# Optimization experiments

Hardware: AMD Instinct MI355X
Metric: run time of the kernel (lower is better)

## Reference

```python
import jax, jax.numpy as jnp
import numpy as np
from jax import lax

ALPHA = 1.5
DIM = -1
N_ITER = 50


def entmax_bisect(x, alpha=ALPHA, dim=DIM, n_iter=N_ITER):
    # alpha == 1.0 would reduce to softmax; alpha is a static Python float here.
    if alpha == 1.0:
        return jax.nn.softmax(x, axis=dim)
    am1 = alpha - 1.0
    z = x - jnp.max(x, axis=dim, keepdims=True)          # max(z) == 0 along dim
    am1_z = am1 * z
    # torch code sorts z and takes the top element; that equals max(z) == 0, so
    # hi = 0 and lo = hi - 1. We compute the max directly (same math, no sort).
    hi = jnp.max(am1_z, axis=dim, keepdims=True)          # == 0
    lo = hi - 1.0

    inv_am1 = 1.0 / am1

    def sum_probs(tau):
        # sum_i max(0, am1*z_i - tau)^{1/am1}, keepdims
        diff = jnp.maximum(am1_z - tau, 0.0)
        return jnp.sum(jnp.power(diff, inv_am1), axis=dim, keepdims=True)

    # The torch version expands lo downward (up to 64 times) until
    # sum_probs(lo) >= 1 everywhere. Since max(am1_z) == hi, at lo = hi - 1 the
    # argmax element alone contributes (hi - lo)^{1/am1} = 1^{1/am1} = 1, so
    # sum_probs(lo) >= 1 always holds and the torch loop breaks on the first
    # iteration without ever modifying lo. We therefore skip it (identical math).

    def bisect_step(carry, _):
        lo, hi = carry
        mid = (lo + hi) * 0.5
        s = sum_probs(mid)
        lo = jnp.where(s > 1.0, mid, lo)
        hi = jnp.where(s <= 1.0, mid, hi)
        return (lo, hi), None

    (lo, hi), _ = lax.scan(bisect_step, (lo, hi), None, length=n_iter)
    tau_star = (lo + hi) * 0.5
    p = jnp.power(jnp.maximum(am1_z - tau_star, 0.0), inv_am1)
    return p / jnp.maximum(jnp.sum(p, axis=dim, keepdims=True), 1e-12)


def setup_inputs() -> dict:
    key = jax.random.key(0)
    x = jax.random.normal(key, (8, 2048, 2048), dtype=jnp.float32)
    return {"x": x}


def reference(x):
    return entmax_bisect(x, alpha=ALPHA, dim=DIM, n_iter=N_ITER)
```

## Files before the change

### kernel.cpp

```cpp
#include <hip/hip_runtime.h>


constexpr int N = 2048;
constexpr int PER_LANE = N / 64;
constexpr int WAVES_PER_BLOCK = 4;
constexpr int K1 = 6;
constexpr int TOTAL_ITER = 50;
constexpr int BMAX = 8;

__global__ __launch_bounds__(256, 4)
void entmax15_kernel(const float* __restrict__ x,
                     float* __restrict__ out, int rows) {
    __shared__ float s_buf[WAVES_PER_BLOCK][BMAX];
    __shared__ int   s_cnt[WAVES_PER_BLOCK];

    const int wave = threadIdx.x >> 6;
    const int lane = threadIdx.x & 63;
    const int row  = blockIdx.x * WAVES_PER_BLOCK + wave;
    if (row >= rows) return;

    const float4* xr   = reinterpret_cast<const float4*>(x   + (size_t)row * N);
    float4*       outr = reinterpret_cast<float4*>(out + (size_t)row * N);

    float v[PER_LANE];
    #pragma unroll
    for (int c = 0; c < PER_LANE / 4; ++c) {
        float4 t = xr[lane + 64 * c];
        v[4*c+0] = t.x; v[4*c+1] = t.y; v[4*c+2] = t.z; v[4*c+3] = t.w;
    }

    float m = v[0];
    #pragma unroll
    for (int i = 1; i < PER_LANE; ++i) m = fmaxf(m, v[i]);
    #pragma unroll
    for (int off = 32; off >= 1; off >>= 1)
        m = fmaxf(m, __shfl_xor(m, off, 64));

    const float nhm = -0.5f * m;
    #pragma unroll
    for (int i = 0; i < PER_LANE; ++i) v[i] = fmaf(0.5f, v[i], nhm);

    float lo = -1.0f, hi = 0.0f;

    for (int it = 0; it < K1; ++it) {
        const float mid = 0.5f * (lo + hi);
        float s0 = 0.f, s1_ = 0.f, s2_ = 0.f, s3_ = 0.f;
        #pragma unroll
        for (int i = 0; i < PER_LANE; i += 4) {
            float d0 = fmaxf(v[i+0] - mid, 0.f);
            float d1 = fmaxf(v[i+1] - mid, 0.f);
            float d2 = fmaxf(v[i+2] - mid, 0.f);
            float d3 = fmaxf(v[i+3] - mid, 0.f);
            s0 = fmaf(d0, d0, s0); s1_ = fmaf(d1, d1, s1_);
            s2_ = fmaf(d2, d2, s2_); s3_ = fmaf(d3, d3, s3_);
        }
        float s = (s0 + s1_) + (s2_ + s3_);
        #pragma unroll
        for (int off = 32; off >= 1; off >>= 1)
            s += __shfl_xor(s, off, 64);
        if (s > 1.0f) lo = mid; else hi = mid;
    }

    if (lane < BMAX) s_buf[wave][lane] = -1e30f;
    if (lane == 0)   s_cnt[wave] = 0;

    const float cth = hi, lof = lo;
    float nA = 0.f, S1 = 0.f, S2 = 0.f;
    #pragma unroll
    for (int i = 0; i < PER_LANE; ++i) {
        float u  = v[i] - cth;
        float um = fmaxf(u, 0.f);
        nA += (u > 0.f) ? 1.0f : 0.0f;
        S1 += um;
        S2 = fmaf(um, um, S2);
        if (u <= 0.f && v[i] > lof) {
            int k = atomicAdd(&s_cnt[wave], 1);
            if (k < BMAX) s_buf[wave][k] = v[i];
        }
    }
    #pragma unroll
    for (int off = 32; off >= 1; off >>= 1) {
        nA += __shfl_xor(nA, off, 64);
        S1 += __shfl_xor(S1, off, 64);
        S2 += __shfl_xor(S2, off, 64);
    }

    const int cnt = s_cnt[wave];
    float b0 = s_buf[wave][0], b1 = s_buf[wave][1];
    float b2 = s_buf[wave][2], b3 = s_buf[wave][3];
    float b4 = s_buf[wave][4], b5 = s_buf[wave][5];
    float b6 = s_buf[wave][6], b7 = s_buf[wave][7];

    float tau;
    bool fast = (cnt <= BMAX);
    if (fast) {
        #define CE(a, b) { float _t = fmaxf(a, b); b = fminf(a, b); a = _t; }
        CE(b0,b1) CE(b2,b3) CE(b4,b5) CE(b6,b7)
        CE(b0,b2) CE(b1,b3) CE(b4,b6) CE(b5,b7)
        CE(b1,b2) CE(b5,b6)
        CE(b0,b4) CE(b1,b5) CE(b2,b6) CE(b3,b7)
        CE(b2,b4) CE(b3,b5)
        CE(b1,b2) CE(b3,b4) CE(b5,b6)
        #undef CE

        float nk = nA, S1k = S1, S2k = S2;
        #define STEP(bk) {                                                  \
            float t_  = bk - cth;                                           \
            float sc_ = fmaf(t_, fmaf(nk, t_, -2.0f * S1k), S2k);           \
            bool  ac_ = sc_ < 1.0f;                                         \
            float ta_ = ac_ ? t_ : 0.0f;                                    \
            nk  += ac_ ? 1.0f : 0.0f;                                       \
            S1k += ta_;                                                     \
            S2k  = fmaf(ta_, ta_, S2k); }
        STEP(b0) STEP(b1) STEP(b2) STEP(b3)
        STEP(b4) STEP(b5) STEP(b6) STEP(b7)
        #undef STEP

        float disc = fmaxf(fmaf(S1k, S1k, -nk * (S2k - 1.0f)), 0.0f);
        float t = (S1k - sqrtf(disc)) / nk;
        tau = cth + t;
    } else {
        for (int it = 0; it < TOTAL_ITER - K1; ++it) {
            const float mid = 0.5f * (lo + hi);
            float s0 = 0.f, s1_ = 0.f, s2_ = 0.f, s3_ = 0.f;
            #pragma unroll
            for (int i = 0; i < PER_LANE; i += 4) {
                float d0 = fmaxf(v[i+0] - mid, 0.f);
                float d1 = fmaxf(v[i+1] - mid, 0.f);
                float d2 = fmaxf(v[i+2] - mid, 0.f);
                float d3 = fmaxf(v[i+3] - mid, 0.f);
                s0 = fmaf(d0, d0, s0); s1_ = fmaf(d1, d1, s1_);
                s2_ = fmaf(d2, d2, s2_); s3_ = fmaf(d3, d3, s3_);
            }
            float s = (s0 + s1_) + (s2_ + s3_);
            #pragma unroll
            for (int off = 32; off >= 1; off >>= 1)
                s += __shfl_xor(s, off, 64);
            if (s > 1.0f) lo = mid; else hi = mid;
        }
        tau = 0.5f * (lo + hi);
    }

    float s0 = 0.f, s1_ = 0.f, s2_ = 0.f, s3_ = 0.f;
    #pragma unroll
    for (int i = 0; i < PER_LANE; i += 4) {
        float d0 = fmaxf(v[i+0] - tau, 0.f);
        float d1 = fmaxf(v[i+1] - tau, 0.f);
        float d2 = fmaxf(v[i+2] - tau, 0.f);
        float d3 = fmaxf(v[i+3] - tau, 0.f);
        v[i+0] = d0 * d0; v[i+1] = d1 * d1;
        v[i+2] = d2 * d2; v[i+3] = d3 * d3;
        s0 += v[i+0]; s1_ += v[i+1]; s2_ += v[i+2]; s3_ += v[i+3];
    }
    float s = (s0 + s1_) + (s2_ + s3_);
    #pragma unroll
    for (int off = 32; off >= 1; off >>= 1)
        s += __shfl_xor(s, off, 64);
    const float inv = 1.0f / fmaxf(s, 1e-12f);

    #pragma unroll
    for (int c = 0; c < PER_LANE / 4; ++c) {
        float4 t;
        t.x = v[4*c+0] * inv;
        t.y = v[4*c+1] * inv;
        t.z = v[4*c+2] * inv;
        t.w = v[4*c+3] * inv;
        outr[lane + 64 * c] = t;
    }
}

extern "C" void kernel_launch(void* const* d_in, const int* in_sizes, int n_in,
                              void* d_out, int out_size, void* d_ws, size_t ws_size,
                              hipStream_t stream) {
    const float* x = (const float*)d_in[0];
    float* out = (float*)d_out;
    const int rows = in_sizes[0] / N;
    const int blocks = (rows + WAVES_PER_BLOCK - 1) / WAVES_PER_BLOCK;
    entmax15_kernel<<<blocks, 64 * WAVES_PER_BLOCK, 0, stream>>>(x, out, rows);
}
```

Measured before the change: 57.32 us.

## Compact support candidates into per-lane LDS list before bisection

Each lane writes the elements that can possibly be in the support (v > -1) into a small per-lane shared-memory candidate buffer. The bisection steps, the boundary search and the normalisation sum then run over at most 12 candidates per lane instead of 32 values, falling back to the full 50-step bisection if any lane overflows. It also raises launch bounds to 6 blocks per CU, recomputes the output from v at store time, and uses nontemporal stores. The price is more LDS use per block (about 12 KB) and extra shared writes and reads.

```diff
diff --git a/kernel.cpp b/kernel.cpp
--- a/kernel.cpp
+++ b/kernel.cpp
@@ -1,126 +1,168 @@
 #include <hip/hip_runtime.h>
 
+
+typedef float f32x4 __attribute__((ext_vector_type(4)));
 
 constexpr int N = 2048;
 constexpr int PER_LANE = N / 64;
-constexpr int WAVES_PER_BLOCK = 4;
+constexpr int WPB = 4;
+constexpr int CAPL = 12;
+constexpr int BMAX = 8;
 constexpr int K1 = 6;
 constexpr int TOTAL_ITER = 50;
-constexpr int BMAX = 8;
-
-__global__ __launch_bounds__(256, 4)
+
+__device__ __forceinline__ float wave_sum(float s) {
+    #pragma unroll
+    for (int off = 32; off >= 1; off >>= 1)
+        s += __shfl_xor(s, off, 64);
+    return s;
+}
+__device__ __forceinline__ float wave_max(float m) {
+    #pragma unroll
+    for (int off = 32; off >= 1; off >>= 1)
+        m = fmaxf(m, __shfl_xor(m, off, 64));
+    return m;
+}
+
+__global__ __launch_bounds__(256, 6)
 void entmax15_kernel(const float* __restrict__ x,
                      float* __restrict__ out, int rows) {
-    __shared__ float s_buf[WAVES_PER_BLOCK][BMAX];
-    __shared__ int   s_cnt[WAVES_PER_BLOCK];
+    __shared__ float s_cand[WPB][CAPL][64];
+    __shared__ float s_bnd[WPB][BMAX];
+    __shared__ int   s_cnt[WPB];
 
     const int wave = threadIdx.x >> 6;
     const int lane = threadIdx.x & 63;
-    const int row  = blockIdx.x * WAVES_PER_BLOCK + wave;
+    const int row  = blockIdx.x * WPB + wave;
     if (row >= rows) return;
 
-    const float4* xr   = reinterpret_cast<const float4*>(x   + (size_t)row * N);
-    float4*       outr = reinterpret_cast<float4*>(out + (size_t)row * N);
+    const f32x4* xr   = reinterpret_cast<const f32x4*>(x + (size_t)row * N);
+    f32x4*       outr = reinterpret_cast<f32x4*>(out + (size_t)row * N);
 
     float v[PER_LANE];
     #pragma unroll
     for (int c = 0; c < PER_LANE / 4; ++c) {
-        float4 t = xr[lane + 64 * c];
+        f32x4 t = xr[lane + 64 * c];
         v[4*c+0] = t.x; v[4*c+1] = t.y; v[4*c+2] = t.z; v[4*c+3] = t.w;
     }
 
     float m = v[0];
     #pragma unroll
     for (int i = 1; i < PER_LANE; ++i) m = fmaxf(m, v[i]);
-    #pragma unroll
-    for (int off = 32; off >= 1; off >>= 1)
-        m = fmaxf(m, __shfl_xor(m, off, 64));
+    m = wave_max(m);
 
     const float nhm = -0.5f * m;
     #pragma unroll
     for (int i = 0; i < PER_LANE; ++i) v[i] = fmaf(0.5f, v[i], nhm);
 
-    float lo = -1.0f, hi = 0.0f;
-
-    for (int it = 0; it < K1; ++it) {
-        const float mid = 0.5f * (lo + hi);
-        float s0 = 0.f, s1_ = 0.f, s2_ = 0.f, s3_ = 0.f;
-        #pragma unroll
-        for (int i = 0; i < PER_LANE; i += 4) {
-            float d0 = fmaxf(v[i+0] - mid, 0.f);
-            float d1 = fmaxf(v[i+1] - mid, 0.f);
-            float d2 = fmaxf(v[i+2] - mid, 0.f);
-            float d3 = fmaxf(v[i+3] - mid, 0.f);
-            s0 = fmaf(d0, d0, s0); s1_ = fmaf(d1, d1, s1_);
-            s2_ = fmaf(d2, d2, s2_); s3_ = fmaf(d3, d3, s3_);
-        }
-        float s = (s0 + s1_) + (s2_ + s3_);
-        #pragma unroll
-        for (int off = 32; off >= 1; off >>= 1)
-            s += __shfl_xor(s, off, 64);
-        if (s > 1.0f) lo = mid; else hi = mid;
-    }
-
-    if (lane < BMAX) s_buf[wave][lane] = -1e30f;
+    #pragma unroll
+    for (int k = 0; k < CAPL; ++k) s_cand[wave][k][lane] = -1e30f;
+    if (lane < BMAX) s_bnd[wave][lane] = -1e30f;
     if (lane == 0)   s_cnt[wave] = 0;
 
-    const float cth = hi, lof = lo;
-    float nA = 0.f, S1 = 0.f, S2 = 0.f;
+    int j = 0;
     #pragma unroll
     for (int i = 0; i < PER_LANE; ++i) {
-        float u  = v[i] - cth;
-        float um = fmaxf(u, 0.f);
-        nA += (u > 0.f) ? 1.0f : 0.0f;
-        S1 += um;
-        S2 = fmaf(um, um, S2);
-        if (u <= 0.f && v[i] > lof) {
-            int k = atomicAdd(&s_cnt[wave], 1);
-            if (k < BMAX) s_buf[wave][k] = v[i];
-        }
-    }
-    #pragma unroll
-    for (int off = 32; off >= 1; off >>= 1) {
-        nA += __shfl_xor(nA, off, 64);
-        S1 += __shfl_xor(S1, off, 64);
-        S2 += __shfl_xor(S2, off, 64);
-    }
-
-    const int cnt = s_cnt[wave];
-    float b0 = s_buf[wave][0], b1 = s_buf[wave][1];
-    float b2 = s_buf[wave][2], b3 = s_buf[wave][3];
-    float b4 = s_buf[wave][4], b5 = s_buf[wave][5];
-    float b6 = s_buf[wave][6], b7 = s_buf[wave][7];
-
-    float tau;
-    bool fast = (cnt <= BMAX);
-    if (fast) {
-        #define CE(a, b) { float _t = fmaxf(a, b); b = fminf(a, b); a = _t; }
-        CE(b0,b1) CE(b2,b3) CE(b4,b5) CE(b6,b7)
-        CE(b0,b2) CE(b1,b3) CE(b4,b6) CE(b5,b7)
-        CE(b1,b2) CE(b5,b6)
-        CE(b0,b4) CE(b1,b5) CE(b2,b6) CE(b3,b7)
-        CE(b2,b4) CE(b3,b5)
-        CE(b1,b2) CE(b3,b4) CE(b5,b6)
-        #undef CE
-
-        float nk = nA, S1k = S1, S2k = S2;
-        #define STEP(bk) {                                                  \
-            float t_  = bk - cth;                                           \
-            float sc_ = fmaf(t_, fmaf(nk, t_, -2.0f * S1k), S2k);           \
-            bool  ac_ = sc_ < 1.0f;                                         \
-            float ta_ = ac_ ? t_ : 0.0f;                                    \
-            nk  += ac_ ? 1.0f : 0.0f;                                       \
-            S1k += ta_;                                                     \
-            S2k  = fmaf(ta_, ta_, S2k); }
-        STEP(b0) STEP(b1) STEP(b2) STEP(b3)
-        STEP(b4) STEP(b5) STEP(b6) STEP(b7)
-        #undef STEP
-
-        float disc = fmaxf(fmaf(S1k, S1k, -nk * (S2k - 1.0f)), 0.0f);
-        float t = (S1k - sqrtf(disc)) / nk;
-        tau = cth + t;
+        const bool cand = v[i] > -1.0f;
+        const int  slot = (j < CAPL - 1) ? j : (CAPL - 1);
+        if (cand) s_cand[wave][slot][lane] = v[i];
+        j += cand ? 1 : 0;
+    }
+
+    float tau, ssum;
+    if (!__any(j > CAPL)) {
+        float cd[CAPL];
+        #pragma unroll
+        for (int k = 0; k < CAPL; ++k) cd[k] = s_cand[wave][k][lane];
+
+        float lo = -1.0f, hi = 0.0f;
+        for (int it = 0; it < K1; ++it) {
+            const float mid = 0.5f * (lo + hi);
+            float sa = 0.f, sb = 0.f;
+            #pragma unroll
+            for (int k = 0; k < CAPL; k += 2) {
+                float d0 = fmaxf(cd[k]   - mid, 0.f);
+                float d1 = fmaxf(cd[k+1] - mid, 0.f);
+                sa = fmaf(d0, d0, sa);
+                sb = fmaf(d1, d1, sb);
+            }
+            float s = wave_sum(sa + sb);
+            if (s > 1.0f) lo = mid; else hi = mid;
+        }
+
+        const float cth = hi, lof = lo;
+        float nA = 0.f, S1 = 0.f, S2 = 0.f;
+        #pragma unroll
+        for (int k = 0; k < CAPL; ++k) {
+            float u  = cd[k] - cth;
+            float um = fmaxf(u, 0.f);
+            nA += (u > 0.f) ? 1.0f : 0.0f;
+            S1 += um;
+            S2  = fmaf(um, um, S2);
+            if (u <= 0.f && cd[k] > lof) {
+                int t = atomicAdd(&s_cnt[wave], 1);
+                if (t < BMAX) s_bnd[wave][t] = cd[k];
+            }
+        }
+        nA = wave_sum(nA); S1 = wave_sum(S1); S2 = wave_sum(S2);
+
+        const int cnt = s_cnt[wave];
+        if (cnt <= BMAX) {
+            float b0 = s_bnd[wave][0], b1 = s_bnd[wave][1];
+            float b2 = s_bnd[wave][2], b3 = s_bnd[wave][3];
+            float b4 = s_bnd[wave][4], b5 = s_bnd[wave][5];
+            float b6 = s_bnd[wave][6], b7 = s_bnd[wave][7];
+            #define CE(a, b) { float _t = fmaxf(a, b); b = fminf(a, b); a = _t; }
+            CE(b0,b1) CE(b2,b3) CE(b4,b5) CE(b6,b7)
+            CE(b0,b2) CE(b1,b3) CE(b4,b6) CE(b5,b7)
+            CE(b1,b2) CE(b5,b6)
+            CE(b0,b4) CE(b1,b5) CE(b2,b6) CE(b3,b7)
+            CE(b2,b4) CE(b3,b5)
+            CE(b1,b2) CE(b3,b4) CE(b5,b6)
+            #undef CE
+            float nk = nA, S1k = S1, S2k = S2;
+            #define STEP(bk) {                                              \
+                float t_  = bk - cth;                                       \
+                float sc_ = fmaf(t_, fmaf(nk, t_, -2.0f * S1k), S2k);       \
+                bool  ac_ = sc_ < 1.0f;                                     \
+                float ta_ = ac_ ? t_ : 0.0f;                                \
+                nk  += ac_ ? 1.0f : 0.0f;                                   \
+                S1k += ta_;                                                 \
+                S2k  = fmaf(ta_, ta_, S2k); }
+            STEP(b0) STEP(b1) STEP(b2) STEP(b3)
+            STEP(b4) STEP(b5) STEP(b6) STEP(b7)
+            #undef STEP
+            float disc = fmaxf(fmaf(S1k, S1k, -nk * (S2k - 1.0f)), 0.0f);
+            tau = cth + (S1k - sqrtf(disc)) / nk;
+        } else {
+            for (int it = 0; it < TOTAL_ITER - K1; ++it) {
+                const float mid = 0.5f * (lo + hi);
+                float sa = 0.f, sb = 0.f;
+                #pragma unroll
+                for (int k = 0; k < CAPL; k += 2) {
+                    float d0 = fmaxf(cd[k]   - mid, 0.f);
+                    float d1 = fmaxf(cd[k+1] - mid, 0.f);
+                    sa = fmaf(d0, d0, sa);
+                    sb = fmaf(d1, d1, sb);
+                }
+                float s = wave_sum(sa + sb);
+                if (s > 1.0f) lo = mid; else hi = mid;
+            }
+            tau = 0.5f * (lo + hi);
+        }
+
+        float sa = 0.f, sb = 0.f;
+        #pragma unroll
+        for (int k = 0; k < CAPL; k += 2) {
+            float d0 = fmaxf(cd[k]   - tau, 0.f);
+            float d1 = fmaxf(cd[k+1] - tau, 0.f);
+            sa = fmaf(d0, d0, sa);
+            sb = fmaf(d1, d1, sb);
+        }
+        ssum = wave_sum(sa + sb);
     } else {
-        for (int it = 0; it < TOTAL_ITER - K1; ++it) {
+        float lo = -1.0f, hi = 0.0f;
+        for (int it = 0; it < TOTAL_ITER; ++it) {
             const float mid = 0.5f * (lo + hi);
             float s0 = 0.f, s1_ = 0.f, s2_ = 0.f, s3_ = 0.f;
             #pragma unroll
@@ -132,40 +174,32 @@
                 s0 = fmaf(d0, d0, s0); s1_ = fmaf(d1, d1, s1_);
                 s2_ = fmaf(d2, d2, s2_); s3_ = fmaf(d3, d3, s3_);
             }
-            float s = (s0 + s1_) + (s2_ + s3_);
-            #pragma unroll
-            for (int off = 32; off >= 1; off >>= 1)
-                s += __shfl_xor(s, off, 64);
+            float s = wave_sum((s0 + s1_) + (s2_ + s3_));
             if (s > 1.0f) lo = mid; else hi = mid;
         }
         tau = 0.5f * (lo + hi);
-    }
-
-    float s0 = 0.f, s1_ = 0.f, s2_ = 0.f, s3_ = 0.f;
-    #pragma unroll
-    for (int i = 0; i < PER_LANE; i += 4) {
-        float d0 = fmaxf(v[i+0] - tau, 0.f);
-        float d1 = fmaxf(v[i+1] - tau, 0.f);
-        float d2 = fmaxf(v[i+2] - tau, 0.f);
-        float d3 = fmaxf(v[i+3] - tau, 0.f);
-        v[i+0] = d0 * d0; v[i+1] = d1 * d1;
-        v[i+2] = d2 * d2; v[i+3] = d3 * d3;
-        s0 += v[i+0]; s1_ += v[i+1]; s2_ += v[i+2]; s3_ += v[i+3];
-    }
-    float s = (s0 + s1_) + (s2_ + s3_);
-    #pragma unroll
-    for (int off = 32; off >= 1; off >>= 1)
-        s += __shfl_xor(s, off, 64);
-    const float inv = 1.0f / fmaxf(s, 1e-12f);
-
+        float s0 = 0.f;
+        #pragma unroll
+        for (int i = 0; i < PER_LANE; ++i) {
+            float d = fmaxf(v[i] - tau, 0.f);
+            s0 = fmaf(d, d, s0);
+        }
+        ssum = wave_sum(s0);
+    }
+
+    const float inv = 1.0f / fmaxf(ssum, 1e-12f);
     #pragma unroll
     for (int c = 0; c < PER_LANE / 4; ++c) {
-        float4 t;
-        t.x = v[4*c+0] * inv;
-        t.y = v[4*c+1] * inv;
-        t.z = v[4*c+2] * inv;
-        t.w = v[4*c+3] * inv;
-        outr[lane + 64 * c] = t;
+        float d0 = fmaxf(v[4*c+0] - tau, 0.f);
+        float d1 = fmaxf(v[4*c+1] - tau, 0.f);
+        float d2 = fmaxf(v[4*c+2] - tau, 0.f);
+        float d3 = fmaxf(v[4*c+3] - tau, 0.f);
+        f32x4 t;
+        t.x = (d0 * d0) * inv;
+        t.y = (d1 * d1) * inv;
+        t.z = (d2 * d2) * inv;
+        t.w = (d3 * d3) * inv;
+        __builtin_nontemporal_store(t, &outr[lane + 64 * c]);
     }
 }
 
@@ -175,6 +209,6 @@
     const float* x = (const float*)d_in[0];
     float* out = (float*)d_out;
     const int rows = in_sizes[0] / N;
-    const int blocks = (rows + WAVES_PER_BLOCK - 1) / WAVES_PER_BLOCK;
-    entmax15_kernel<<<blocks, 64 * WAVES_PER_BLOCK, 0, stream>>>(x, out, rows);
-}
+    const int blocks = (rows + WPB - 1) / WPB;
+    entmax15_kernel<<<blocks, 64 * WPB, 0, stream>>>(x, out, rows);
+}
```

Result: no change. 57.75 us (+0.8%).
